# Optimization experiments

Hardware: AMD Instinct MI355X
Metric: run time of the kernel (lower is better)

## Reference

```python
import jax, jax.numpy as jnp
import numpy as np

EPS = 1e-6


def _mp_cos_pointwise(p, q, M2):
    # p, q: [B, L, K]; M2: [C, K] (squared perspective weights)
    # cosine between (p*M_c) and (q*M_c) along K, per channel c -> [B, L, C]
    num = jnp.einsum('blk,blk,ck->blc', p, q, M2)
    pn = jnp.sqrt(jnp.maximum(jnp.einsum('blk,ck->blc', p * p, M2), EPS))
    qn = jnp.sqrt(jnp.maximum(jnp.einsum('blk,ck->blc', q * q, M2), EPS))
    return num / pn / qn


def setup_inputs() -> dict:
    key = jax.random.key(0)
    ks = jax.random.split(key, 10)
    B, Lq, Ld, K, C = 32, 200, 200, 200, 50
    f32 = jnp.float32
    def unif(k, shape):  # keras 'uniform' init: U(-0.05, 0.05)
        return jax.random.uniform(k, shape, f32, -0.05, 0.05)
    return {
        'q_rep': jax.random.normal(ks[0], (B, Lq, K), f32),
        'q_last': jax.random.normal(ks[1], (B, K), f32),
        'q_mask': jnp.ones((B, Lq), f32),
        'd_rep': jax.random.normal(ks[2], (B, Ld, K), f32),
        'd_last': jax.random.normal(ks[3], (B, K), f32),
        'd_mask': jnp.ones((B, Ld), f32),
        'full_M': unif(ks[4], (C, K)),
        'maxpool_M': unif(ks[5], (C, K)),
        'att_M': unif(ks[6], (C, K)),
        'max_att_M': unif(ks[7], (C, K)),
    }


def reference(q_rep, q_last, q_mask, d_rep, d_last, d_mask,
              full_M, maxpool_M, att_M, max_att_M):
    outputs = []

    # relevancy matrix: cosine(q[b,j,:], d[b,i,:]) -> [B, Ld, Lq]
    num = jnp.einsum('bik,bjk->bij', d_rep, q_rep)
    dn = jnp.sqrt(jnp.maximum(jnp.sum(d_rep * d_rep, -1), EPS))  # [B, Ld]
    qn = jnp.sqrt(jnp.maximum(jnp.sum(q_rep * q_rep, -1), EPS))  # [B, Lq]
    rel = num / qn[:, None, :] / dn[:, :, None]
    rel = rel * q_mask[:, None, :] * d_mask[:, :, None]

    # full matching: cosine(d[b,i]*M_c, q_last[b]*M_c) -> [B, Ld, C]
    M2 = full_M * full_M
    fnum = jnp.einsum('bik,bk,ck->bic', d_rep, q_last, M2)
    fpn = jnp.sqrt(jnp.maximum(jnp.einsum('bik,ck->bic', d_rep * d_rep, M2), EPS))
    fqn = jnp.sqrt(jnp.maximum(jnp.einsum('bk,ck->bc', q_last * q_last, M2), EPS))
    outputs.append(fnum / fpn / fqn[:, None, :])

    # maxpool matching: cosine(d[b,i]*M_c, q[b,j]*M_c) -> [B, Ld, Lq, C]
    M2 = maxpool_M * maxpool_M
    mnum = jnp.einsum('bik,bjk,ck->bijc', d_rep, q_rep, M2)
    mpn = jnp.sqrt(jnp.maximum(jnp.einsum('bik,ck->bic', d_rep * d_rep, M2), EPS))
    mqn = jnp.sqrt(jnp.maximum(jnp.einsum('bjk,ck->bjc', q_rep * q_rep, M2), EPS))
    mm = mnum / mpn[:, :, None, :] / mqn[:, None, :, :]
    outputs.append(jnp.concatenate([jnp.max(mm, axis=2), jnp.mean(mm, axis=2)], axis=2))

    # attentive matching: cosine-weighted q rep (no softmax -> normalize by sum)
    wq = jnp.einsum('bij,bjk->bik', rel, q_rep)
    wq = wq / (jnp.sum(rel, axis=-1) + EPS)[..., None]  # [B, Ld, K]
    outputs.append(_mp_cos_pointwise(d_rep, wq, att_M * att_M))

    # max-attentive matching: gather best-matching q word per d position
    idx = jnp.argmax(rel, axis=2)  # [B, Ld]
    max_q = jnp.take_along_axis(q_rep, idx[:, :, None], axis=1)  # [B, Ld, K]
    outputs.append(_mp_cos_pointwise(d_rep, max_q, max_att_M * max_att_M))

    return jnp.concatenate(outputs, axis=-1)  # [B, Ld, 5*C]
```

## Files before the change

### kernel.cpp

```cpp
#include <hip/hip_runtime.h>
#include <math.h>


#define EPS 1e-6f
#define NEG_HUGE -3.4e38f

typedef __bf16 bf16x8 __attribute__((ext_vector_type(8)));
typedef float f32x16 __attribute__((ext_vector_type(16)));

constexpr size_t OFF_M2ALL = 0;
constexpr size_t OFF_M2B16 = 40000;
constexpr size_t OFF_QB16  = 63296;
constexpr size_t OFF_DB16  = 915264;
constexpr size_t OFF_INVFPN= 1767232;
constexpr size_t OFF_INVMPN= 2087232;
constexpr size_t OFF_INVAPN= 2407232;
constexpr size_t OFF_INVXPN= 2727232;
constexpr size_t OFF_INVMQN= 3047232;
constexpr size_t OFF_INVXQN= 3367232;
constexpr size_t OFF_INVFQN= 3687232;
constexpr size_t OFF_INVDN = 3688832;
constexpr size_t OFF_INVQN = 3695232;
constexpr size_t OFF_IDX   = 3701632;
constexpr size_t OFF_WQ    = 3708032;
constexpr size_t OFF_G     = 4988032;
constexpr size_t OFF_PMAX2 = 6268032;
constexpr size_t OFF_PSUM2 = 6677632;

__global__ __launch_bounds__(256) void k_prep(
    const float* __restrict__ qR, const float* __restrict__ dR,
    const float* __restrict__ fM, const float* __restrict__ mM,
    const float* __restrict__ aM, const float* __restrict__ xM,
    unsigned short* __restrict__ qb16, unsigned short* __restrict__ db16,
    float* __restrict__ invdn, float* __restrict__ invqn,
    float* __restrict__ m2all, unsigned short* __restrict__ m2b16)
{
  int blk = blockIdx.x;
  int tid = threadIdx.x;
  if (blk < 4096) {
    int task = blk*4 + (tid >> 6);
    int l = tid & 63;
    int isQ = task >= 8192;
    int r = isQ ? task - 8192 : task;
    int b = r >> 8, j = r & 255;
    unsigned short* dst = (isQ ? qb16 : db16) + (size_t)r*208;
    if (j < 200) {
      const float* src = (isQ ? qR : dR) + (size_t)(b*200 + j)*200;
      float4 v = {0.f,0.f,0.f,0.f};
      if (l < 50) v = *(const float4*)(src + l*4);
      float s = fmaf(v.x,v.x, fmaf(v.y,v.y, fmaf(v.z,v.z, v.w*v.w)));
#pragma unroll
      for (int m = 32; m; m >>= 1) s += __shfl_xor(s, m);
      if (l == 0) {
        float rr = rsqrtf(fmaxf(s, EPS));
        if (isQ) invqn[b*200 + j] = rr; else invdn[b*200 + j] = rr;
      }
      if (l < 52) {
        ushort4 o = {0,0,0,0};
        if (l < 50) {
          __bf16 h0=(__bf16)v.x, h1=(__bf16)v.y, h2=(__bf16)v.z, h3=(__bf16)v.w;
          o.x = *(unsigned short*)&h0; o.y = *(unsigned short*)&h1;
          o.z = *(unsigned short*)&h2; o.w = *(unsigned short*)&h3;
        }
        *(ushort4*)(dst + l*4) = o;
      }
    } else {
      if (l < 52) { ushort4 z = {0,0,0,0}; *(ushort4*)(dst + l*4) = z; }
    }
  } else {
    int i = (blk - 4096)*256 + tid;
    if (i < 40000) {
      int m = i / 10000, r = i % 10000;
      const float* s = (m==0)?fM:(m==1)?mM:(m==2)?aM:xM;
      float v = s[r];
      m2all[i] = v*v;
    }
    if (i < 224*208) {
      int row = i / 208, k = i % 208;
      unsigned short o = 0;
      if (row < 200 && k < 200) {
        int m = row / 50, c = row % 50;
        const float* s = (m==0)?fM:(m==1)?mM:(m==2)?aM:xM;
        float v = s[c*200 + k];
        __bf16 h = (__bf16)(v*v);
        o = *(unsigned short*)&h;
      }
      m2b16[i] = o;
    }
  }
}

__global__ __launch_bounds__(256) void k_mid(
    const float* __restrict__ dR, const float* __restrict__ qR,
    const float* __restrict__ qL, const unsigned short* __restrict__ m2b16,
    float* __restrict__ invfpn, float* __restrict__ invmpn,
    float* __restrict__ invapn, float* __restrict__ invxpn,
    float* __restrict__ invmqn, float* __restrict__ invxqn,
    float* __restrict__ invfqn,
    const float* __restrict__ qMask, const float* __restrict__ dMask,
    const float* __restrict__ invdn, const float* __restrict__ invqn,
    float* __restrict__ wq, int* __restrict__ idxout)
{
  int tid = threadIdx.x;
  if (blockIdx.x < 702) {
    int w = tid >> 6, lane = tid & 63;
    int n = lane & 31, h = lane >> 5;
    int task = blockIdx.x*4 + w;
    if (task >= 2807) return;
    int rt = task / 7, nt = task % 7;
    int row = rt*32 + n;

    const float* src;
    if (row < 6400)       src = dR + (size_t)row*200;
    else if (row < 12800) src = qR + (size_t)(row-6400)*200;
    else                  src = qL + (size_t)(row-12800)*200;

    bf16x8 afrag[13];
#pragma unroll
    for (int ks = 0; ks < 13; ks++) {
      int ko = ks*16 + h*8;
      bf16x8 af;
      if (ko < 200) {
        float4 a0 = *(const float4*)(src + ko);
        float4 a1 = *(const float4*)(src + ko + 4);
        af[0] = (__bf16)(a0.x*a0.x); af[1] = (__bf16)(a0.y*a0.y);
        af[2] = (__bf16)(a0.z*a0.z); af[3] = (__bf16)(a0.w*a0.w);
        af[4] = (__bf16)(a1.x*a1.x); af[5] = (__bf16)(a1.y*a1.y);
        af[6] = (__bf16)(a1.z*a1.z); af[7] = (__bf16)(a1.w*a1.w);
      } else {
#pragma unroll
        for (int z = 0; z < 8; z++) af[z] = (__bf16)0.0f;
      }
      afrag[ks] = af;
    }

    f32x16 C;
#pragma unroll
    for (int z = 0; z < 16; z++) C[z] = 0.f;
    const unsigned short* bp = m2b16 + (size_t)(nt*32 + n)*208 + h*8;
#pragma unroll
    for (int ks = 0; ks < 13; ks++) {
      bf16x8 bf = *(const bf16x8*)(bp + ks*16);
      C = __builtin_amdgcn_mfma_f32_32x32x16_bf16(afrag[ks], bf, C, 0, 0, 0);
    }

    int cp = nt*32 + n;
    if (cp < 200) {
      int m = cp / 50, c = cp % 50;
#pragma unroll
      for (int r = 0; r < 16; r++) {
        int grow = rt*32 + (r & 3) + 8*(r >> 2) + 4*h;
        float v = rsqrtf(fmaxf(C[r], EPS));
        if (grow < 6400) {
          if (m == 0)      invfpn[grow*50 + c] = v;
          else if (m == 1) invmpn[grow*50 + c] = v;
          else if (m == 2) invapn[grow*50 + c] = v;
          else             invxpn[grow*50 + c] = v;
        } else if (grow < 12800) {
          int r2 = grow - 6400;
          if (m == 1)      invmqn[c*6400 + r2] = v;
          else if (m == 3) invxqn[r2*50 + c] = v;
        } else {
          if (m == 0)      invfqn[(grow-12800)*50 + c] = v;
        }
      }
    }
  } else {
    __shared__ float relsh[8][256];
    __shared__ float redv[4][8][2];
    __shared__ int   redi[4][8];
    __shared__ float invrs_sh[8];
    int blk = blockIdx.x - 702;
    int b  = blk / 25;
    int i0 = (blk % 25) * 8;
    int j = tid, jr = min(j, 199);
    bool jv = j < 200;
    const float* qb = qR + b*40000;
    const float* db = dR + (b*200 + i0)*200;
    float acc[8];
#pragma unroll
    for (int ii = 0; ii < 8; ii++) acc[ii] = 0.f;

    const float* qrow = qb + jr*200;
    for (int k4 = 0; k4 < 200; k4 += 4) {
      float4 qv = *(const float4*)(qrow + k4);
#pragma unroll
      for (int ii = 0; ii < 8; ii++) {
        acc[ii] = fmaf(db[ii*200 + k4 + 0], qv.x, acc[ii]);
        acc[ii] = fmaf(db[ii*200 + k4 + 1], qv.y, acc[ii]);
        acc[ii] = fmaf(db[ii*200 + k4 + 2], qv.z, acc[ii]);
        acc[ii] = fmaf(db[ii*200 + k4 + 3], qv.w, acc[ii]);
      }
    }

    float iqn = invqn[b*200 + jr];
    float qm  = qMask[b*200 + jr];
    int w = tid >> 6, l = tid & 63;
    float rv[8];
#pragma unroll
    for (int ii = 0; ii < 8; ii++) {
      float idn = invdn[b*200 + i0 + ii];
      float dm  = dMask[b*200 + i0 + ii];
      float r = acc[ii]*iqn*idn*qm*dm;
      rv[ii] = r;
      relsh[ii][j] = jv ? r : 0.f;
    }
#pragma unroll
    for (int ii = 0; ii < 8; ii++) {
      float vm = jv ? rv[ii] : NEG_HUGE;
      float vs = jv ? rv[ii] : 0.f;
      int bj = jr;
#pragma unroll
      for (int m = 32; m; m >>= 1) {
        float ov = __shfl_xor(vm, m);
        int   oj = __shfl_xor(bj, m);
        vs += __shfl_xor(vs, m);
        if (ov > vm || (ov == vm && oj < bj)) { vm = ov; bj = oj; }
      }
      if (l == 0) { redv[w][ii][0] = vm; redv[w][ii][1] = vs; redi[w][ii] = bj; }
    }
    __syncthreads();
    if (tid < 8) {
      float bv = redv[0][tid][0], ss = redv[0][tid][1]; int bj = redi[0][tid];
      for (int w2 = 1; w2 < 4; w2++) {
        ss += redv[w2][tid][1];
        float wv = redv[w2][tid][0]; int wj = redi[w2][tid];
        if (wv > bv || (wv == bv && wj < bj)) { bv = wv; bj = wj; }
      }
      invrs_sh[tid] = 1.f/(ss + EPS);
      idxout[b*200 + i0 + tid] = bj;
    }
    __syncthreads();

    int kl = min(tid, 199); bool kv = tid < 200;
    float acw[8];
#pragma unroll
    for (int ii = 0; ii < 8; ii++) acw[ii] = 0.f;
    for (int j0 = 0; j0 < 200; j0 += 4) {
      float qv0 = qb[(j0+0)*200 + kl];
      float qv1 = qb[(j0+1)*200 + kl];
      float qv2 = qb[(j0+2)*200 + kl];
      float qv3 = qb[(j0+3)*200 + kl];
#pragma unroll
      for (int ii = 0; ii < 8; ii++) {
        float4 rs = *(const float4*)&relsh[ii][j0];
        acw[ii] = fmaf(rs.x, qv0, acw[ii]);
        acw[ii] = fmaf(rs.y, qv1, acw[ii]);
        acw[ii] = fmaf(rs.z, qv2, acw[ii]);
        acw[ii] = fmaf(rs.w, qv3, acw[ii]);
      }
    }
#pragma unroll
    for (int ii = 0; ii < 8; ii++) {
      float v = acw[ii]*invrs_sh[ii];
      if (kv) wq[(size_t)(b*200 + i0 + ii)*200 + tid] = v;
    }
  }
}

__global__ __launch_bounds__(512,2) void k_big(
    const unsigned short* __restrict__ db16, const unsigned short* __restrict__ qb16,
    const float* __restrict__ m2all, const float* __restrict__ invmqn,
    float* __restrict__ pmax2, float* __restrict__ psum2,
    const float* __restrict__ dR, const float* __restrict__ qR,
    const float* __restrict__ qL, const float* __restrict__ wq,
    const int* __restrict__ idx, const unsigned short* __restrict__ m2b16,
    float* __restrict__ G)
{
  int tid = threadIdx.x;
  int w = tid >> 6, lane = tid & 63;
  int n = lane & 31, h = lane >> 5;
  if (blockIdx.x < 1600) {
    __shared__ __align__(16) unsigned short qsh[128*216];
    int b = blockIdx.x / 50, c = blockIdx.x % 50;
    const float* M2 = m2all + 10000 + c*200;
    const unsigned short* dbp = db16 + (size_t)(b*256 + w*32 + n)*208 + h*8;

    bf16x8 afrag[13];
#pragma unroll
    for (int ks = 0; ks < 13; ks++) afrag[ks] = *(const bf16x8*)(dbp + ks*16);

    float vm[16], vs[16];
#pragma unroll
    for (int r = 0; r < 16; r++) { vm[r] = NEG_HUGE; vs[r] = 0.f; }

    for (int jh = 0; jh < 2; jh++) {
      int nrows = jh ? 96 : 128;
      int njt   = jh ? 3 : 4;
      __syncthreads();
      {
        const unsigned short* src = qb16 + (size_t)(b*256 + jh*128)*208;
        const float* iqb = invmqn + c*6400 + b*200;
        for (int s = tid; s < nrows*26; s += 512) {
          int r = s / 26, ch = s - r*26;
          int j = jh*128 + r;
          float iq = (j < 200) ? iqb[j] : 0.f;
          int k0 = ch*8;
          bf16x8 v = *(const bf16x8*)(src + (size_t)r*208 + k0);
          float4 m0 = *(const float4*)(M2 + k0);
          float4 m1 = *(const float4*)(M2 + k0 + 4);
          bf16x8 o;
          o[0] = (__bf16)((float)v[0]*iq*m0.x); o[1] = (__bf16)((float)v[1]*iq*m0.y);
          o[2] = (__bf16)((float)v[2]*iq*m0.z); o[3] = (__bf16)((float)v[3]*iq*m0.w);
          o[4] = (__bf16)((float)v[4]*iq*m1.x); o[5] = (__bf16)((float)v[5]*iq*m1.y);
          o[6] = (__bf16)((float)v[6]*iq*m1.z); o[7] = (__bf16)((float)v[7]*iq*m1.w);
          *(bf16x8*)(qsh + r*216 + k0) = o;
        }
      }
      __syncthreads();

      for (int jt = 0; jt < njt; jt++) {
        f32x16 C;
#pragma unroll
        for (int z = 0; z < 16; z++) C[z] = 0.f;
        const unsigned short* bptr = qsh + (jt*32 + n)*216 + h*8;
#pragma unroll
        for (int ks = 0; ks < 13; ks++) {
          bf16x8 bf = *(const bf16x8*)(bptr + ks*16);
          C = __builtin_amdgcn_mfma_f32_32x32x16_bf16(afrag[ks], bf, C, 0, 0, 0);
        }
        bool jv = (jh*128 + jt*32 + n) < 200;
#pragma unroll
        for (int r = 0; r < 16; r++) {
          vm[r] = fmaxf(vm[r], jv ? C[r] : NEG_HUGE);
          vs[r] += C[r];
        }
      }
    }

#pragma unroll
    for (int r = 0; r < 16; r++) {
      float a = vm[r], s = vs[r];
#pragma unroll
      for (int m = 1; m <= 16; m <<= 1) {
        a = fmaxf(a, __shfl_xor(a, m));
        s += __shfl_xor(s, m);
      }
      vm[r] = a; vs[r] = s;
    }
    if (n == 0) {
#pragma unroll
      for (int r = 0; r < 16; r++) {
        int i = w*32 + (r & 3) + 8*(r >> 2) + 4*h;
        pmax2[(size_t)blockIdx.x*256 + i] = vm[r];
        psum2[(size_t)blockIdx.x*256 + i] = vs[r];
      }
    }
  } else {
    int task = (blockIdx.x - 1600)*8 + w;
    int mp = task / 400;
    int sub = task % 400;
    int rt = sub >> 1, nt = sub & 1;
    int row = rt*32 + n;
    int bb = row / 200;
    int msel = (mp == 0) ? 0 : (mp == 3) ? 3 : 2;

    const float* s0 = dR + (size_t)row*200;
    const float* s1;
    if (mp == 0)      s1 = qL + (size_t)bb*200;
    else if (mp == 1) s1 = wq + (size_t)row*200;
    else if (mp == 2) { s0 = wq + (size_t)row*200; s1 = s0; }
    else              s1 = qR + (size_t)(bb*200 + idx[row])*200;

    bf16x8 afrag[13];
#pragma unroll
    for (int ks = 0; ks < 13; ks++) {
      int ko = ks*16 + h*8;
      bf16x8 af;
      if (ko < 200) {
        float4 a0 = *(const float4*)(s0 + ko);
        float4 a1 = *(const float4*)(s0 + ko + 4);
        float4 b0 = *(const float4*)(s1 + ko);
        float4 b1 = *(const float4*)(s1 + ko + 4);
        af[0] = (__bf16)(a0.x*b0.x); af[1] = (__bf16)(a0.y*b0.y);
        af[2] = (__bf16)(a0.z*b0.z); af[3] = (__bf16)(a0.w*b0.w);
        af[4] = (__bf16)(a1.x*b1.x); af[5] = (__bf16)(a1.y*b1.y);
        af[6] = (__bf16)(a1.z*b1.z); af[7] = (__bf16)(a1.w*b1.w);
      } else {
#pragma unroll
        for (int z = 0; z < 8; z++) af[z] = (__bf16)0.0f;
      }
      afrag[ks] = af;
    }

    f32x16 C;
#pragma unroll
    for (int z = 0; z < 16; z++) C[z] = 0.f;
    const unsigned short* bp = m2b16 + (size_t)(msel*50 + nt*32 + n)*208 + h*8;
#pragma unroll
    for (int ks = 0; ks < 13; ks++) {
      bf16x8 bf = *(const bf16x8*)(bp + ks*16);
      C = __builtin_amdgcn_mfma_f32_32x32x16_bf16(afrag[ks], bf, C, 0, 0, 0);
    }
    int cc = nt*32 + n;
    if (cc < 50) {
#pragma unroll
      for (int r = 0; r < 16; r++) {
        int mrow = (r & 3) + 8*(r >> 2) + 4*h;
        G[(size_t)(mp*6400 + rt*32 + mrow)*50 + cc] = C[r];
      }
    }
  }
}

__global__ void k_out(
    const float* __restrict__ G, const float* __restrict__ pmax2,
    const float* __restrict__ psum2, const float* __restrict__ invfpn,
    const float* __restrict__ invmpn, const float* __restrict__ invapn,
    const float* __restrict__ invxpn, const float* __restrict__ invfqn,
    const float* __restrict__ invxqn, const int* __restrict__ idx,
    float* __restrict__ out)
{
  int row = blockIdx.x;
  int l = threadIdx.x;
  if (l >= 250) return;
  int b = row / 200, i = row % 200;
  int seg = l / 50, c = l % 50;
  float o;
  if (seg == 0) {
    o = G[(size_t)(0*6400 + row)*50 + c] * invfpn[row*50 + c] * invfqn[b*50 + c];
  } else if (seg == 1) {
    o = pmax2[(size_t)(b*50 + c)*256 + i] * invmpn[row*50 + c];
  } else if (seg == 2) {
    o = psum2[(size_t)(b*50 + c)*256 + i] * invmpn[row*50 + c] * (1.f/200.f);
  } else if (seg == 3) {
    o = G[(size_t)(1*6400 + row)*50 + c] * invapn[row*50 + c]
        * rsqrtf(fmaxf(G[(size_t)(2*6400 + row)*50 + c], EPS));
  } else {
    int jid = idx[row];
    o = G[(size_t)(3*6400 + row)*50 + c] * invxpn[row*50 + c]
        * invxqn[(b*200 + jid)*50 + c];
  }
  out[(size_t)row*250 + l] = o;
}

extern "C" void kernel_launch(void* const* d_in, const int* in_sizes, int n_in,
                              void* d_out, int out_size, void* d_ws, size_t ws_size,
                              hipStream_t stream) {
  const float* qR = (const float*)d_in[0];
  const float* qL = (const float*)d_in[1];
  const float* qM = (const float*)d_in[2];
  const float* dR = (const float*)d_in[3];
  const float* dM = (const float*)d_in[5];
  const float* fullM = (const float*)d_in[6];
  const float* mpM   = (const float*)d_in[7];
  const float* attM  = (const float*)d_in[8];
  const float* xM    = (const float*)d_in[9];

  float* ws  = (float*)d_ws;
  float* out = (float*)d_out;

  float* m2all  = ws + OFF_M2ALL;
  unsigned short* m2b16 = (unsigned short*)(ws + OFF_M2B16);
  unsigned short* qb16 = (unsigned short*)(ws + OFF_QB16);
  unsigned short* db16 = (unsigned short*)(ws + OFF_DB16);
  float* invfpn = ws + OFF_INVFPN;
  float* invmpn = ws + OFF_INVMPN;
  float* invapn = ws + OFF_INVAPN;
  float* invxpn = ws + OFF_INVXPN;
  float* invmqn = ws + OFF_INVMQN;
  float* invxqn = ws + OFF_INVXQN;
  float* invfqn = ws + OFF_INVFQN;
  float* invdn  = ws + OFF_INVDN;
  float* invqn  = ws + OFF_INVQN;
  int*   idxp   = (int*)(ws + OFF_IDX);
  float* wqp    = ws + OFF_WQ;
  float* G      = ws + OFF_G;
  float* pmax2  = ws + OFF_PMAX2;
  float* psum2  = ws + OFF_PSUM2;

  k_prep<<<4278, 256, 0, stream>>>(qR, dR, fullM, mpM, attM, xM,
                                   qb16, db16, invdn, invqn, m2all, m2b16);
  k_mid<<<1502, 256, 0, stream>>>(dR, qR, qL, m2b16,
                                  invfpn, invmpn, invapn, invxpn,
                                  invmqn, invxqn, invfqn,
                                  qM, dM, invdn, invqn, wqp, idxp);
  k_big<<<1800, 512, 0, stream>>>(db16, qb16, m2all, invmqn, pmax2, psum2,
                                  dR, qR, qL, wqp, idxp, m2b16, G);
  k_out<<<6400, 256, 0, stream>>>(G, pmax2, psum2, invfpn, invmpn, invapn,
                                  invxpn, invfqn, invxqn, idxp, out);
}
```

Baseline: 248.1 us.

## Merge prep and mid kernels into one front kernel, recompute norms locally

Fuses the bf16 conversion/prep kernel and the mid kernel (relevancy/attention and MFMA perspective norms) into a single k_front launch with 512-thread blocks. This removes one launch and the dependency between them. To break that dependency, the relevancy blocks now compute the q and d inverse norms themselves in shared memory, and the MFMA norm blocks square the M weights inline instead of reading the prepacked m2b16. This adds redundant work: each relevancy unit recomputes all 200 q norms, and the per-block shared memory footprint grows.

```diff
diff --git a/kernel.cpp b/kernel.cpp
--- a/kernel.cpp
+++ b/kernel.cpp
@@ -19,27 +19,226 @@
 constexpr size_t OFF_INVMQN= 3047232;
 constexpr size_t OFF_INVXQN= 3367232;
 constexpr size_t OFF_INVFQN= 3687232;
-constexpr size_t OFF_INVDN = 3688832;
-constexpr size_t OFF_INVQN = 3695232;
 constexpr size_t OFF_IDX   = 3701632;
 constexpr size_t OFF_WQ    = 3708032;
 constexpr size_t OFF_G     = 4988032;
 constexpr size_t OFF_PMAX2 = 6268032;
 constexpr size_t OFF_PSUM2 = 6677632;
 
-__global__ __launch_bounds__(256) void k_prep(
+struct RWShared {
+  float relsh[2][8][256];
+  float iqn[2][200];
+  float idn[2][8];
+  float redv[2][4][8][2];
+  int   redi[2][4][8];
+  float invrs[2][8];
+};
+
+__global__ __launch_bounds__(512) void k_front(
     const float* __restrict__ qR, const float* __restrict__ dR,
+    const float* __restrict__ qL,
+    const float* __restrict__ qMask, const float* __restrict__ dMask,
     const float* __restrict__ fM, const float* __restrict__ mM,
     const float* __restrict__ aM, const float* __restrict__ xM,
     unsigned short* __restrict__ qb16, unsigned short* __restrict__ db16,
-    float* __restrict__ invdn, float* __restrict__ invqn,
-    float* __restrict__ m2all, unsigned short* __restrict__ m2b16)
+    float* __restrict__ m2all, unsigned short* __restrict__ m2b16,
+    float* __restrict__ invfpn, float* __restrict__ invmpn,
+    float* __restrict__ invapn, float* __restrict__ invxpn,
+    float* __restrict__ invmqn, float* __restrict__ invxqn,
+    float* __restrict__ invfqn,
+    float* __restrict__ wq, int* __restrict__ idxout)
 {
+  __shared__ RWShared sh;
+  int tid = threadIdx.x;
   int blk = blockIdx.x;
-  int tid = threadIdx.x;
-  if (blk < 4096) {
-    int task = blk*4 + (tid >> 6);
-    int l = tid & 63;
+  int w = tid >> 6, lane = tid & 63;
+  int n = lane & 31, h = lane >> 5;
+
+  if (blk < 400) {
+    int u = tid >> 8;
+    int tid2 = tid & 255;
+    int unit = blk*2 + u;
+    int b = unit / 25, i0 = (unit % 25)*8;
+    int w2 = tid2 >> 6, l = lane;
+    int j = tid2, jr = min(j, 199);
+    bool jv = j < 200;
+    const float* qb = qR + b*40000;
+    const float* db = dR + (b*200 + i0)*200;
+
+    for (int jq = w2*50; jq < w2*50 + 50; jq++) {
+      float4 v = {0.f,0.f,0.f,0.f};
+      if (l < 50) v = *(const float4*)(qb + jq*200 + l*4);
+      float s = fmaf(v.x,v.x, fmaf(v.y,v.y, fmaf(v.z,v.z, v.w*v.w)));
+#pragma unroll
+      for (int m = 32; m; m >>= 1) s += __shfl_xor(s, m);
+      if (l == 0) sh.iqn[u][jq] = rsqrtf(fmaxf(s, EPS));
+    }
+    if (w2 == 0) {
+      for (int ii = 0; ii < 8; ii++) {
+        float4 v = {0.f,0.f,0.f,0.f};
+        if (l < 50) v = *(const float4*)(db + ii*200 + l*4);
+        float s = fmaf(v.x,v.x, fmaf(v.y,v.y, fmaf(v.z,v.z, v.w*v.w)));
+#pragma unroll
+        for (int m = 32; m; m >>= 1) s += __shfl_xor(s, m);
+        if (l == 0) sh.idn[u][ii] = rsqrtf(fmaxf(s, EPS));
+      }
+    }
+    __syncthreads();
+
+    float acc[8];
+#pragma unroll
+    for (int ii = 0; ii < 8; ii++) acc[ii] = 0.f;
+    const float* qrow = qb + jr*200;
+    for (int k4 = 0; k4 < 200; k4 += 4) {
+      float4 qv = *(const float4*)(qrow + k4);
+#pragma unroll
+      for (int ii = 0; ii < 8; ii++) {
+        acc[ii] = fmaf(db[ii*200 + k4 + 0], qv.x, acc[ii]);
+        acc[ii] = fmaf(db[ii*200 + k4 + 1], qv.y, acc[ii]);
+        acc[ii] = fmaf(db[ii*200 + k4 + 2], qv.z, acc[ii]);
+        acc[ii] = fmaf(db[ii*200 + k4 + 3], qv.w, acc[ii]);
+      }
+    }
+    float iqnv = sh.iqn[u][jr];
+    float qm  = qMask[b*200 + jr];
+    float rv[8];
+#pragma unroll
+    for (int ii = 0; ii < 8; ii++) {
+      float idnv = sh.idn[u][ii];
+      float dm = dMask[b*200 + i0 + ii];
+      float r = acc[ii]*iqnv*idnv*qm*dm;
+      rv[ii] = r;
+      sh.relsh[u][ii][j] = jv ? r : 0.f;
+    }
+#pragma unroll
+    for (int ii = 0; ii < 8; ii++) {
+      float vmv = jv ? rv[ii] : NEG_HUGE;
+      float vsv = jv ? rv[ii] : 0.f;
+      int bj = jr;
+#pragma unroll
+      for (int m = 32; m; m >>= 1) {
+        float ov = __shfl_xor(vmv, m);
+        int   oj = __shfl_xor(bj, m);
+        vsv += __shfl_xor(vsv, m);
+        if (ov > vmv || (ov == vmv && oj < bj)) { vmv = ov; bj = oj; }
+      }
+      if (l == 0) { sh.redv[u][w2][ii][0] = vmv; sh.redv[u][w2][ii][1] = vsv; sh.redi[u][w2][ii] = bj; }
+    }
+    __syncthreads();
+    if (tid2 < 8) {
+      float bv = sh.redv[u][0][tid2][0], ss = sh.redv[u][0][tid2][1];
+      int bj = sh.redi[u][0][tid2];
+      for (int w3 = 1; w3 < 4; w3++) {
+        ss += sh.redv[u][w3][tid2][1];
+        float wv = sh.redv[u][w3][tid2][0]; int wj = sh.redi[u][w3][tid2];
+        if (wv > bv || (wv == bv && wj < bj)) { bv = wv; bj = wj; }
+      }
+      sh.invrs[u][tid2] = 1.f/(ss + EPS);
+      idxout[b*200 + i0 + tid2] = bj;
+    }
+    __syncthreads();
+    int kl = min(tid2, 199); bool kv = tid2 < 200;
+    float acw[8];
+#pragma unroll
+    for (int ii = 0; ii < 8; ii++) acw[ii] = 0.f;
+    for (int j0 = 0; j0 < 200; j0 += 4) {
+      float qv0 = qb[(j0+0)*200 + kl];
+      float qv1 = qb[(j0+1)*200 + kl];
+      float qv2 = qb[(j0+2)*200 + kl];
+      float qv3 = qb[(j0+3)*200 + kl];
+#pragma unroll
+      for (int ii = 0; ii < 8; ii++) {
+        float4 rs = *(const float4*)&sh.relsh[u][ii][j0];
+        acw[ii] = fmaf(rs.x, qv0, acw[ii]);
+        acw[ii] = fmaf(rs.y, qv1, acw[ii]);
+        acw[ii] = fmaf(rs.z, qv2, acw[ii]);
+        acw[ii] = fmaf(rs.w, qv3, acw[ii]);
+      }
+    }
+#pragma unroll
+    for (int ii = 0; ii < 8; ii++) {
+      float v = acw[ii]*sh.invrs[u][ii];
+      if (kv) wq[(size_t)(b*200 + i0 + ii)*200 + tid2] = v;
+    }
+  } else if (blk < 751) {
+    int task = (blk - 400)*8 + w;
+    if (task < 2807) {
+      int rt = task / 7, nt = task % 7;
+      int row = rt*32 + n;
+      const float* src;
+      if (row < 6400)       src = dR + (size_t)row*200;
+      else if (row < 12800) src = qR + (size_t)(row-6400)*200;
+      else                  src = qL + (size_t)(row-12800)*200;
+
+      bf16x8 afrag[13];
+#pragma unroll
+      for (int ks = 0; ks < 13; ks++) {
+        int ko = ks*16 + h*8;
+        bf16x8 af;
+        if (ko < 200) {
+          float4 a0 = *(const float4*)(src + ko);
+          float4 a1 = *(const float4*)(src + ko + 4);
+          af[0]=(__bf16)(a0.x*a0.x); af[1]=(__bf16)(a0.y*a0.y);
+          af[2]=(__bf16)(a0.z*a0.z); af[3]=(__bf16)(a0.w*a0.w);
+          af[4]=(__bf16)(a1.x*a1.x); af[5]=(__bf16)(a1.y*a1.y);
+          af[6]=(__bf16)(a1.z*a1.z); af[7]=(__bf16)(a1.w*a1.w);
+        } else {
+#pragma unroll
+          for (int z = 0; z < 8; z++) af[z] = (__bf16)0.0f;
+        }
+        afrag[ks] = af;
+      }
+      int cp = nt*32 + n;
+      bool cpv = cp < 200;
+      int mIdx = 0, cIdx = 0;
+      const float* msrc = fM;
+      if (cpv) {
+        mIdx = cp / 50; cIdx = cp % 50;
+        msrc = ((mIdx==0)?fM:(mIdx==1)?mM:(mIdx==2)?aM:xM) + cIdx*200;
+      }
+      f32x16 C;
+#pragma unroll
+      for (int z = 0; z < 16; z++) C[z] = 0.f;
+#pragma unroll
+      for (int ks = 0; ks < 13; ks++) {
+        int ko = ks*16 + h*8;
+        bf16x8 bf;
+        if (cpv && ko < 200) {
+          float4 b0 = *(const float4*)(msrc + ko);
+          float4 b1 = *(const float4*)(msrc + ko + 4);
+          bf[0]=(__bf16)(b0.x*b0.x); bf[1]=(__bf16)(b0.y*b0.y);
+          bf[2]=(__bf16)(b0.z*b0.z); bf[3]=(__bf16)(b0.w*b0.w);
+          bf[4]=(__bf16)(b1.x*b1.x); bf[5]=(__bf16)(b1.y*b1.y);
+          bf[6]=(__bf16)(b1.z*b1.z); bf[7]=(__bf16)(b1.w*b1.w);
+        } else {
+#pragma unroll
+          for (int z = 0; z < 8; z++) bf[z] = (__bf16)0.0f;
+        }
+        C = __builtin_amdgcn_mfma_f32_32x32x16_bf16(afrag[ks], bf, C, 0, 0, 0);
+      }
+      if (cpv) {
+#pragma unroll
+        for (int r = 0; r < 16; r++) {
+          int grow = rt*32 + (r & 3) + 8*(r >> 2) + 4*h;
+          float v = rsqrtf(fmaxf(C[r], EPS));
+          if (grow < 6400) {
+            if (mIdx == 0)      invfpn[grow*50 + cIdx] = v;
+            else if (mIdx == 1) invmpn[grow*50 + cIdx] = v;
+            else if (mIdx == 2) invapn[grow*50 + cIdx] = v;
+            else                invxpn[grow*50 + cIdx] = v;
+          } else if (grow < 12800) {
+            int r2 = grow - 6400;
+            if (mIdx == 1)      invmqn[cIdx*6400 + r2] = v;
+            else if (mIdx == 3) invxqn[r2*50 + cIdx] = v;
+          } else {
+            if (mIdx == 0)      invfqn[(grow-12800)*50 + cIdx] = v;
+          }
+        }
+      }
+    }
+  } else if (blk < 2799) {
+    int task = (blk - 751)*8 + w;
+    int l = lane;
     int isQ = task >= 8192;
     int r = isQ ? task - 8192 : task;
     int b = r >> 8, j = r & 255;
@@ -48,13 +247,6 @@
       const float* src = (isQ ? qR : dR) + (size_t)(b*200 + j)*200;
       float4 v = {0.f,0.f,0.f,0.f};
       if (l < 50) v = *(const float4*)(src + l*4);
-      float s = fmaf(v.x,v.x, fmaf(v.y,v.y, fmaf(v.z,v.z, v.w*v.w)));
-#pragma unroll
-      for (int m = 32; m; m >>= 1) s += __shfl_xor(s, m);
-      if (l == 0) {
-        float rr = rsqrtf(fmaxf(s, EPS));
-        if (isQ) invqn[b*200 + j] = rr; else invdn[b*200 + j] = rr;
-      }
       if (l < 52) {
         ushort4 o = {0,0,0,0};
         if (l < 50) {
@@ -68,7 +260,7 @@
       if (l < 52) { ushort4 z = {0,0,0,0}; *(ushort4*)(dst + l*4) = z; }
     }
   } else {
-    int i = (blk - 4096)*256 + tid;
+    int i = (blk - 2799)*512 + tid;
     if (i < 40000) {
       int m = i / 10000, r = i % 10000;
       const float* s = (m==0)?fM:(m==1)?mM:(m==2)?aM:xM;
@@ -82,178 +274,10 @@
         int m = row / 50, c = row % 50;
         const float* s = (m==0)?fM:(m==1)?mM:(m==2)?aM:xM;
         float v = s[c*200 + k];
-        __bf16 h = (__bf16)(v*v);
-        o = *(unsigned short*)&h;
+        __bf16 hh = (__bf16)(v*v);
+        o = *(unsigned short*)&hh;
       }
       m2b16[i] = o;
-    }
-  }
-}
-
-__global__ __launch_bounds__(256) void k_mid(
-    const float* __restrict__ dR, const float* __restrict__ qR,
-    const float* __restrict__ qL, const unsigned short* __restrict__ m2b16,
-    float* __restrict__ invfpn, float* __restrict__ invmpn,
-    float* __restrict__ invapn, float* __restrict__ invxpn,
-    float* __restrict__ invmqn, float* __restrict__ invxqn,
-    float* __restrict__ invfqn,
-    const float* __restrict__ qMask, const float* __restrict__ dMask,
-    const float* __restrict__ invdn, const float* __restrict__ invqn,
-    float* __restrict__ wq, int* __restrict__ idxout)
-{
-  int tid = threadIdx.x;
-  if (blockIdx.x < 702) {
-    int w = tid >> 6, lane = tid & 63;
-    int n = lane & 31, h = lane >> 5;
-    int task = blockIdx.x*4 + w;
-    if (task >= 2807) return;
-    int rt = task / 7, nt = task % 7;
-    int row = rt*32 + n;
-
-    const float* src;
-    if (row < 6400)       src = dR + (size_t)row*200;
-    else if (row < 12800) src = qR + (size_t)(row-6400)*200;
-    else                  src = qL + (size_t)(row-12800)*200;
-
-    bf16x8 afrag[13];
-#pragma unroll
-    for (int ks = 0; ks < 13; ks++) {
-      int ko = ks*16 + h*8;
-      bf16x8 af;
-      if (ko < 200) {
-        float4 a0 = *(const float4*)(src + ko);
-        float4 a1 = *(const float4*)(src + ko + 4);
-        af[0] = (__bf16)(a0.x*a0.x); af[1] = (__bf16)(a0.y*a0.y);
-        af[2] = (__bf16)(a0.z*a0.z); af[3] = (__bf16)(a0.w*a0.w);
-        af[4] = (__bf16)(a1.x*a1.x); af[5] = (__bf16)(a1.y*a1.y);
-        af[6] = (__bf16)(a1.z*a1.z); af[7] = (__bf16)(a1.w*a1.w);
-      } else {
-#pragma unroll
-        for (int z = 0; z < 8; z++) af[z] = (__bf16)0.0f;
-      }
-      afrag[ks] = af;
-    }
-
-    f32x16 C;
-#pragma unroll
-    for (int z = 0; z < 16; z++) C[z] = 0.f;
-    const unsigned short* bp = m2b16 + (size_t)(nt*32 + n)*208 + h*8;
-#pragma unroll
-    for (int ks = 0; ks < 13; ks++) {
-      bf16x8 bf = *(const bf16x8*)(bp + ks*16);
-      C = __builtin_amdgcn_mfma_f32_32x32x16_bf16(afrag[ks], bf, C, 0, 0, 0);
-    }
-
-    int cp = nt*32 + n;
-    if (cp < 200) {
-      int m = cp / 50, c = cp % 50;
-#pragma unroll
-      for (int r = 0; r < 16; r++) {
-        int grow = rt*32 + (r & 3) + 8*(r >> 2) + 4*h;
-        float v = rsqrtf(fmaxf(C[r], EPS));
-        if (grow < 6400) {
-          if (m == 0)      invfpn[grow*50 + c] = v;
-          else if (m == 1) invmpn[grow*50 + c] = v;
-          else if (m == 2) invapn[grow*50 + c] = v;
-          else             invxpn[grow*50 + c] = v;
-        } else if (grow < 12800) {
-          int r2 = grow - 6400;
-          if (m == 1)      invmqn[c*6400 + r2] = v;
-          else if (m == 3) invxqn[r2*50 + c] = v;
-        } else {
-          if (m == 0)      invfqn[(grow-12800)*50 + c] = v;
-        }
-      }
-    }
-  } else {
-    __shared__ float relsh[8][256];
-    __shared__ float redv[4][8][2];
-    __shared__ int   redi[4][8];
-    __shared__ float invrs_sh[8];
-    int blk = blockIdx.x - 702;
-    int b  = blk / 25;
-    int i0 = (blk % 25) * 8;
-    int j = tid, jr = min(j, 199);
-    bool jv = j < 200;
-    const float* qb = qR + b*40000;
-    const float* db = dR + (b*200 + i0)*200;
-    float acc[8];
-#pragma unroll
-    for (int ii = 0; ii < 8; ii++) acc[ii] = 0.f;
-
-    const float* qrow = qb + jr*200;
-    for (int k4 = 0; k4 < 200; k4 += 4) {
-      float4 qv = *(const float4*)(qrow + k4);
-#pragma unroll
-      for (int ii = 0; ii < 8; ii++) {
-        acc[ii] = fmaf(db[ii*200 + k4 + 0], qv.x, acc[ii]);
-        acc[ii] = fmaf(db[ii*200 + k4 + 1], qv.y, acc[ii]);
-        acc[ii] = fmaf(db[ii*200 + k4 + 2], qv.z, acc[ii]);
-        acc[ii] = fmaf(db[ii*200 + k4 + 3], qv.w, acc[ii]);
-      }
-    }
-
-    float iqn = invqn[b*200 + jr];
-    float qm  = qMask[b*200 + jr];
-    int w = tid >> 6, l = tid & 63;
-    float rv[8];
-#pragma unroll
-    for (int ii = 0; ii < 8; ii++) {
-      float idn = invdn[b*200 + i0 + ii];
-      float dm  = dMask[b*200 + i0 + ii];
-      float r = acc[ii]*iqn*idn*qm*dm;
-      rv[ii] = r;
-      relsh[ii][j] = jv ? r : 0.f;
-    }
-#pragma unroll
-    for (int ii = 0; ii < 8; ii++) {
-      float vm = jv ? rv[ii] : NEG_HUGE;
-      float vs = jv ? rv[ii] : 0.f;
-      int bj = jr;
-#pragma unroll
-      for (int m = 32; m; m >>= 1) {
-        float ov = __shfl_xor(vm, m);
-        int   oj = __shfl_xor(bj, m);
-        vs += __shfl_xor(vs, m);
-        if (ov > vm || (ov == vm && oj < bj)) { vm = ov; bj = oj; }
-      }
-      if (l == 0) { redv[w][ii][0] = vm; redv[w][ii][1] = vs; redi[w][ii] = bj; }
-    }
-    __syncthreads();
-    if (tid < 8) {
-      float bv = redv[0][tid][0], ss = redv[0][tid][1]; int bj = redi[0][tid];
-      for (int w2 = 1; w2 < 4; w2++) {
-        ss += redv[w2][tid][1];
-        float wv = redv[w2][tid][0]; int wj = redi[w2][tid];
-        if (wv > bv || (wv == bv && wj < bj)) { bv = wv; bj = wj; }
-      }
-      invrs_sh[tid] = 1.f/(ss + EPS);
-      idxout[b*200 + i0 + tid] = bj;
-    }
-    __syncthreads();
-
-    int kl = min(tid, 199); bool kv = tid < 200;
-    float acw[8];
-#pragma unroll
-    for (int ii = 0; ii < 8; ii++) acw[ii] = 0.f;
-    for (int j0 = 0; j0 < 200; j0 += 4) {
-      float qv0 = qb[(j0+0)*200 + kl];
-      float qv1 = qb[(j0+1)*200 + kl];
-      float qv2 = qb[(j0+2)*200 + kl];
-      float qv3 = qb[(j0+3)*200 + kl];
-#pragma unroll
-      for (int ii = 0; ii < 8; ii++) {
-        float4 rs = *(const float4*)&relsh[ii][j0];
-        acw[ii] = fmaf(rs.x, qv0, acw[ii]);
-        acw[ii] = fmaf(rs.y, qv1, acw[ii]);
-        acw[ii] = fmaf(rs.z, qv2, acw[ii]);
-        acw[ii] = fmaf(rs.w, qv3, acw[ii]);
-      }
-    }
-#pragma unroll
-    for (int ii = 0; ii < 8; ii++) {
-      float v = acw[ii]*invrs_sh[ii];
-      if (kv) wq[(size_t)(b*200 + i0 + ii)*200 + tid] = v;
     }
   }
 }
@@ -461,20 +485,18 @@
   float* invmqn = ws + OFF_INVMQN;
   float* invxqn = ws + OFF_INVXQN;
   float* invfqn = ws + OFF_INVFQN;
-  float* invdn  = ws + OFF_INVDN;
-  float* invqn  = ws + OFF_INVQN;
   int*   idxp   = (int*)(ws + OFF_IDX);
   float* wqp    = ws + OFF_WQ;
   float* G      = ws + OFF_G;
   float* pmax2  = ws + OFF_PMAX2;
   float* psum2  = ws + OFF_PSUM2;
 
-  k_prep<<<4278, 256, 0, stream>>>(qR, dR, fullM, mpM, attM, xM,
-                                   qb16, db16, invdn, invqn, m2all, m2b16);
-  k_mid<<<1502, 256, 0, stream>>>(dR, qR, qL, m2b16,
-                                  invfpn, invmpn, invapn, invxpn,
-                                  invmqn, invxqn, invfqn,
-                                  qM, dM, invdn, invqn, wqp, idxp);
+  k_front<<<2890, 512, 0, stream>>>(qR, dR, qL, qM, dM,
+                                    fullM, mpM, attM, xM,
+                                    qb16, db16, m2all, m2b16,
+                                    invfpn, invmpn, invapn, invxpn,
+                                    invmqn, invxqn, invfqn,
+                                    wqp, idxp);
   k_big<<<1800, 512, 0, stream>>>(db16, qb16, m2all, invmqn, pmax2, psum2,
                                   dR, qR, qL, wqp, idxp, m2b16, G);
   k_out<<<6400, 256, 0, stream>>>(G, pmax2, psum2, invfpn, invmpn, invapn,
```

After: 331.6 us. +33.7%, slower.
